# Performance work log

Hardware: AMD Instinct MI355X
Metric: run time of the kernel (lower is better)

The kernel has to match this reference:

```python
import jax, jax.numpy as jnp
import numpy as np

TOP_K = 8
N_GROUP = 8
TOPK_GROUP = 4
ROUTED_SCALING = 2.5
NORM_TOPK_PROB = True


def setup_inputs() -> dict:
    key = jax.random.key(0)
    k1, k2, k3 = jax.random.split(key, 3)
    bsz, seq_len, h = 4, 4096, 4096
    n_experts = 256
    hidden_states = jax.random.normal(k1, (bsz, seq_len, h), dtype=jnp.float32)
    # kaiming_uniform_(a=sqrt(5)) -> uniform(-1/sqrt(h), 1/sqrt(h)) approximately
    bound = 1.0 / np.sqrt(h)
    weight = jax.random.uniform(k2, (n_experts, h), dtype=jnp.float32, minval=-bound, maxval=bound)
    # correction bias is a buffer, zero-init; give it small random values to exercise the path
    e_score_correction_bias = jax.random.normal(k3, (n_experts,), dtype=jnp.float32) * 0.01
    return {"hidden_states": hidden_states, "weight": weight,
            "e_score_correction_bias": e_score_correction_bias}


def reference(hidden_states, weight, e_score_correction_bias):
    bsz, seq_len, h = hidden_states.shape
    n_experts = weight.shape[0]
    x = hidden_states.reshape(-1, h).astype(jnp.float32)          # [N, h]
    logits = jnp.einsum('nh,eh->ne', x, weight.astype(jnp.float32))  # [N, E]
    scores = jax.nn.sigmoid(logits)                                # [N, E]
    scores_for_choice = scores + e_score_correction_bias[None, :]  # [N, E]

    # group-limited routing: score each group by sum of its top-2 expert scores
    grouped = scores_for_choice.reshape(-1, N_GROUP, n_experts // N_GROUP)
    group_scores = jax.lax.top_k(grouped, 2)[0].sum(axis=-1)       # [N, G]
    _, group_idx = jax.lax.top_k(group_scores, TOPK_GROUP)         # [N, Kg]
    group_mask = jax.nn.one_hot(group_idx, N_GROUP, dtype=scores.dtype).sum(axis=1)  # [N, G]
    score_mask = jnp.repeat(group_mask, n_experts // N_GROUP, axis=-1)               # [N, E]

    tmp_scores = jnp.where(score_mask > 0, scores_for_choice, 0.0)
    _, topk_idx = jax.lax.top_k(tmp_scores, TOP_K)                 # [N, K]
    topk_weight = jnp.take_along_axis(scores, topk_idx, axis=1)    # [N, K] (no bias)

    if TOP_K > 1 and NORM_TOPK_PROB:
        denom = topk_weight.sum(axis=-1, keepdims=True) + 1e-20
        topk_weight = topk_weight / denom
    topk_weight = topk_weight * ROUTED_SCALING
    return topk_idx, topk_weight
```

## Files before the change

kernel.cpp:

```cpp
#include <hip/hip_runtime.h>
#include <math.h>

#define NTOK 16384
#define H 4096
#define NE 256
#define EPS_E 1.2e-5f
#define EPS_G 2.4e-5f
#define FIXCAP 1024
#define FLAGCAP 8192

typedef __attribute__((ext_vector_type(8))) short short8;
typedef __attribute__((ext_vector_type(4))) float f32x4;

__device__ __forceinline__ unsigned short f2bf(float x) {
    union { float f; unsigned u; } v; v.f = x;
    unsigned r = v.u + 0x7FFF + ((v.u >> 16) & 1);
    return (unsigned short)(r >> 16);
}
__device__ __forceinline__ float bf2f(unsigned short h) {
    union { float f; unsigned u; } v; v.u = ((unsigned)h) << 16;
    return v.f;
}

__global__ void zero_ws(int* ws) { if (threadIdx.x == 0) ws[0] = 0; }

__global__ __launch_bounds__(256)
void split_w(const float* __restrict__ W, unsigned short* __restrict__ whi,
             unsigned short* __restrict__ wlo)
{
    const int i = (blockIdx.x * 256 + threadIdx.x) * 4;
    float4 w4 = *(const float4*)(W + i);
    const float wv[4] = {w4.x, w4.y, w4.z, w4.w};
    ushort4 hh, ll;
    unsigned short* hp = (unsigned short*)&hh;
    unsigned short* lp = (unsigned short*)&ll;
    #pragma unroll
    for (int j = 0; j < 4; ++j) {
        unsigned short h = f2bf(wv[j]);
        hp[j] = h;
        lp[j] = f2bf(wv[j] - bf2f(h));
    }
    *(ushort4*)(whi + i) = hh;
    *(ushort4*)(wlo + i) = ll;
}

__global__ __launch_bounds__(256, 3)
void gemm3(const float* __restrict__ X, const unsigned short* __restrict__ Whi,
           const unsigned short* __restrict__ Wlo, float* __restrict__ logits,
           int m_base)
{
    __shared__ __align__(16) unsigned short smem[24576];
    unsigned short* Ah = smem;
    unsigned short* Al = smem + 4096;
    unsigned short* Bh = smem + 8192;
    unsigned short* Bl = smem + 16384;

    const int t = threadIdx.x;
    const int lane = t & 63;
    const int w = t >> 6;
    const int wm = w >> 1, wn = w & 1;
    const int fr = lane & 15, fq = lane >> 4;

    const int G = (int)gridDim.x;
    const int swz = (blockIdx.x & 7) * (G >> 3) + (blockIdx.x >> 3);
    const int nb = swz & 1;
    const int mb = swz >> 1;
    const int mloc = mb * 64;
    const int m0 = m_base + mloc;
    const int e0 = nb * 128;

    f32x4 acc[2][4];
    #pragma unroll
    for (int a = 0; a < 2; ++a)
        #pragma unroll
        for (int b = 0; b < 4; ++b) acc[a][b] = (f32x4){0.f, 0.f, 0.f, 0.f};

    const int ar = t >> 2;
    const int akc = t & 3;
    const float* gxa = X + (size_t)(m0 + ar) * H + akc * 16;

    const int blr = lane >> 3;
    const int bsrc = (lane & 7) ^ blr;
    const unsigned short* gbh = Whi + (size_t)(e0 + w * 8 + blr) * H + bsrc * 8;
    const unsigned short* gbl = Wlo + (size_t)(e0 + w * 8 + blr) * H + bsrc * 8;

    float4 xr0, xr1, xr2, xr3;
    auto loadX = [&](int kt) {
        const float* p = gxa + (size_t)kt * 64;
        xr0 = *(const float4*)p;       xr1 = *(const float4*)(p + 4);
        xr2 = *(const float4*)(p + 8); xr3 = *(const float4*)(p + 12);
    };

    loadX(0);

    #pragma unroll 1
    for (int kt = 0; kt < 64; ++kt) {
        __builtin_amdgcn_sched_barrier(0);
        __builtin_amdgcn_s_barrier();
        __builtin_amdgcn_sched_barrier(0);
        const size_t k0 = (size_t)kt * 64;
        #pragma unroll
        for (int i = 0; i < 4; ++i) {
            __builtin_amdgcn_global_load_lds(
                (const __attribute__((address_space(1))) void*)(gbh + (size_t)(32 * i) * H + k0),
                (__attribute__((address_space(3))) void*)&Bh[(w * 8 + 32 * i) * 64], 16, 0, 0);
            __builtin_amdgcn_global_load_lds(
                (const __attribute__((address_space(1))) void*)(gbl + (size_t)(32 * i) * H + k0),
                (__attribute__((address_space(3))) void*)&Bl[(w * 8 + 32 * i) * 64], 16, 0, 0);
        }
        __builtin_amdgcn_sched_barrier(0);
        asm volatile("s_waitcnt vmcnt(8)" ::: "memory");
        __builtin_amdgcn_sched_barrier(0);
        {
            const float xf[16] = {xr0.x, xr0.y, xr0.z, xr0.w, xr1.x, xr1.y, xr1.z, xr1.w,
                                  xr2.x, xr2.y, xr2.z, xr2.w, xr3.x, xr3.y, xr3.z, xr3.w};
            short8 h0, h1, l0, l1;
            #pragma unroll
            for (int j = 0; j < 16; ++j) {
                union { float f; unsigned u; } uu; uu.f = xf[j];
                union { unsigned u; float f; } hh; hh.u = uu.u & 0xFFFF0000u;
                union { float f; unsigned u; } ll; ll.f = xf[j] - hh.f;
                unsigned short hs = (unsigned short)(uu.u >> 16);
                unsigned short ls = (unsigned short)(ll.u >> 16);
                if (j < 8) { h0[j] = (short)hs; l0[j] = (short)ls; }
                else       { h1[j - 8] = (short)hs; l1[j - 8] = (short)ls; }
            }
            const int c0 = akc * 2;
            const int p0 = (c0 ^ (ar & 7)) * 8, p1 = ((c0 + 1) ^ (ar & 7)) * 8;
            *(short8*)&Ah[ar * 64 + p0] = h0;
            *(short8*)&Ah[ar * 64 + p1] = h1;
            *(short8*)&Al[ar * 64 + p0] = l0;
            *(short8*)&Al[ar * 64 + p1] = l1;
        }
        loadX(kt + 1 < 64 ? kt + 1 : 63);
        __builtin_amdgcn_sched_barrier(0);
        asm volatile("s_waitcnt vmcnt(4) lgkmcnt(0)" ::: "memory");
        __builtin_amdgcn_sched_barrier(0);
        __builtin_amdgcn_s_barrier();
        __builtin_amdgcn_sched_barrier(0);
        #pragma unroll
        for (int kk = 0; kk < 2; ++kk) {
            short8 ah[2], al[2], bh[4], bl[4];
            #pragma unroll
            for (int mt = 0; mt < 2; ++mt) {
                const int r = wm * 32 + mt * 16 + fr;
                const int pos = ((kk * 4 + fq) ^ (r & 7)) * 8;
                ah[mt] = *(const short8*)&Ah[r * 64 + pos];
                al[mt] = *(const short8*)&Al[r * 64 + pos];
            }
            #pragma unroll
            for (int nt = 0; nt < 4; ++nt) {
                const int r = wn * 64 + nt * 16 + fr;
                const int pos = ((kk * 4 + fq) ^ (r & 7)) * 8;
                bh[nt] = *(const short8*)&Bh[r * 64 + pos];
                bl[nt] = *(const short8*)&Bl[r * 64 + pos];
            }
            #pragma unroll
            for (int mt = 0; mt < 2; ++mt)
                #pragma unroll
                for (int nt = 0; nt < 4; ++nt)
                    acc[mt][nt] = __builtin_amdgcn_mfma_f32_16x16x32_bf16(ah[mt], bh[nt], acc[mt][nt], 0, 0, 0);
            #pragma unroll
            for (int mt = 0; mt < 2; ++mt)
                #pragma unroll
                for (int nt = 0; nt < 4; ++nt)
                    acc[mt][nt] = __builtin_amdgcn_mfma_f32_16x16x32_bf16(ah[mt], bl[nt], acc[mt][nt], 0, 0, 0);
            #pragma unroll
            for (int mt = 0; mt < 2; ++mt)
                #pragma unroll
                for (int nt = 0; nt < 4; ++nt)
                    acc[mt][nt] = __builtin_amdgcn_mfma_f32_16x16x32_bf16(al[mt], bh[nt], acc[mt][nt], 0, 0, 0);
        }
    }
    asm volatile("" :: "v"(xr0.x), "v"(xr1.x), "v"(xr2.x), "v"(xr3.x));

    #pragma unroll
    for (int mt = 0; mt < 2; ++mt)
        #pragma unroll
        for (int nt = 0; nt < 4; ++nt)
            #pragma unroll
            for (int r = 0; r < 4; ++r)
                logits[(size_t)(mloc + wm * 32 + mt * 16 + fq * 4 + r) * NE +
                       (e0 + wn * 64 + nt * 16 + fr)] = acc[mt][nt][r];
}

__global__ __launch_bounds__(256)
void route(const float* __restrict__ logits, const float* __restrict__ bias,
           float* __restrict__ out, int* __restrict__ ws, int cap, int m_base)
{
    const int t = threadIdx.x, lane = t & 63, wv = t >> 6;
    const float4 bf4 = *(const float4*)(bias + lane * 4);
    const float bfa[4] = {bf4.x, bf4.y, bf4.z, bf4.w};

    #pragma unroll 1
    for (int tt = 0; tt < 8; ++tt) {
        const int local = blockIdx.x * 32 + wv * 8 + tt;
        const int n = m_base + local;
        const float4 lg = *(const float4*)&logits[(size_t)local * NE + lane * 4];
        const float lga[4] = {lg.x, lg.y, lg.z, lg.w};
        float s[4], sc[4];
        #pragma unroll
        for (int i = 0; i < 4; ++i) {
            s[i] = 1.f / (1.f + expf(-lga[i]));
            sc[i] = s[i] + bfa[i];
        }
        float a1 = fmaxf(sc[0], sc[1]), a2 = fminf(sc[0], sc[1]);
        float b1 = fmaxf(sc[2], sc[3]), b2 = fminf(sc[2], sc[3]);
        float t1 = fmaxf(a1, b1);
        float t2 = fmaxf(fminf(a1, b1), fmaxf(a2, b2));
        #pragma unroll
        for (int off = 1; off <= 4; off <<= 1) {
            float o1 = __shfl_xor(t1, off, 64);
            float o2 = __shfl_xor(t2, off, 64);
            float n1 = fmaxf(t1, o1);
            float n2 = fmaxf(fminf(t1, o1), fmaxf(t2, o2));
            t1 = n1; t2 = n2;
        }
        const float gsum = t1 + t2;
        float gsv[8];
        #pragma unroll
        for (int g = 0; g < 8; ++g) gsv[g] = __shfl(gsum, g * 8, 64);

        float minsel = 3e38f, maxuns = -3e38f;
        bool sel = false;
        const int myg = lane >> 3;
        #pragma unroll
        for (int g = 0; g < 8; ++g) {
            int cg = 0;
            #pragma unroll
            for (int g2 = 0; g2 < 8; ++g2)
                cg += (gsv[g2] > gsv[g] || (gsv[g2] == gsv[g] && g2 < g)) ? 1 : 0;
            const bool sg = (cg < 4);
            if (sg) minsel = fminf(minsel, gsv[g]); else maxuns = fmaxf(maxuns, gsv[g]);
            if (myg == g) sel = sg;
        }
        bool flag = (minsel - maxuns) < EPS_G;

        float v[4];
        #pragma unroll
        for (int i = 0; i < 4; ++i) v[i] = sel ? sc[i] : 0.f;

        int idxs[8]; float sigs[8];
        float denom = 0.f, prevv = 0.f;
        #pragma unroll
        for (int r = 0; r < 9; ++r) {
            float bv = v[0]; int bi = 0; float bs = s[0];
            #pragma unroll
            for (int i = 1; i < 4; ++i)
                if (v[i] > bv) { bv = v[i]; bi = i; bs = s[i]; }
            int bidx = (lane << 2) + bi;
            #pragma unroll
            for (int off = 1; off < 64; off <<= 1) {
                float ov = __shfl_xor(bv, off, 64);
                int  oi = __shfl_xor(bidx, off, 64);
                float os = __shfl_xor(bs, off, 64);
                if (ov > bv || (ov == bv && oi < bidx)) { bv = ov; bidx = oi; bs = os; }
            }
            if (r > 0) flag = flag || ((prevv - bv) < EPS_E);
            prevv = bv;
            if (r < 8) {
                idxs[r] = bidx; sigs[r] = bs; denom += bs;
                if ((bidx >> 2) == lane) {
                    #pragma unroll
                    for (int i = 0; i < 4; ++i)
                        if ((bidx & 3) == i) v[i] = -3e38f;
                }
            }
        }
        denom += 1e-20f;
        #pragma unroll
        for (int r = 0; r < 8; ++r)
            if (lane == r) {
                out[n * 8 + r] = (float)idxs[r];
                out[NTOK * 8 + n * 8 + r] = sigs[r] / denom * 2.5f;
            }
        if (flag && lane == 0) {
            int slot = atomicAdd(ws, 1);
            if (slot < cap) ws[16 + slot] = n;
        }
    }
}

__global__ __launch_bounds__(256)
void fix1(const float* __restrict__ X, const float* __restrict__ W,
          const int* __restrict__ ws, double* __restrict__ fixlog, int cap)
{
    __shared__ float Xs4[4][4096];
    const int t = threadIdx.x, lane = t & 63, wv = t >> 6;
    int count = ws[0]; if (count > cap) count = cap;
    const int ngrp = (count + 3) >> 2;

    for (int task = blockIdx.x; task < ngrp * 8; task += (int)gridDim.x) {
        const int g = task >> 3, er = task & 7;
        int tok[4];
        #pragma unroll
        for (int q = 0; q < 4; ++q) {
            const int idx = g * 4 + q;
            tok[q] = ws[16 + (idx < count ? idx : g * 4)];
        }
        __syncthreads();
        #pragma unroll
        for (int q = 0; q < 4; ++q)
            for (int k = t * 4; k < 4096; k += 1024)
                *(float4*)&Xs4[q][k] = *(const float4*)(X + (size_t)tok[q] * H + k);
        __syncthreads();
        #pragma unroll 1
        for (int cc = 0; cc < 2; ++cc) {
            const int eb = er * 32 + wv * 8 + cc * 4;
            double a[4][4];
            #pragma unroll
            for (int q = 0; q < 4; ++q)
                #pragma unroll
                for (int ee = 0; ee < 4; ++ee) a[q][ee] = 0.0;
            for (int j = 0; j < 16; ++j) {
                const int kb = (lane + 64 * j) * 4;
                double xx[4][4];
                #pragma unroll
                for (int q = 0; q < 4; ++q) {
                    float4 x4 = *(const float4*)&Xs4[q][kb];
                    xx[q][0] = x4.x; xx[q][1] = x4.y; xx[q][2] = x4.z; xx[q][3] = x4.w;
                }
                #pragma unroll
                for (int ee = 0; ee < 4; ++ee) {
                    float4 w4 = *(const float4*)(W + (size_t)(eb + ee) * H + kb);
                    const double wd[4] = {w4.x, w4.y, w4.z, w4.w};
                    #pragma unroll
                    for (int q = 0; q < 4; ++q)
                        #pragma unroll
                        for (int kq = 0; kq < 4; ++kq)
                            a[q][ee] = fma(xx[q][kq], wd[kq], a[q][ee]);
                }
            }
            #pragma unroll
            for (int q = 0; q < 4; ++q)
                #pragma unroll
                for (int ee = 0; ee < 4; ++ee) {
                    double v = a[q][ee];
                    #pragma unroll
                    for (int off = 1; off < 64; off <<= 1)
                        v += __shfl_xor(v, off, 64);
                    if (lane == 0) fixlog[(size_t)(g * 4 + q) * NE + eb + ee] = v;
                }
        }
    }
}

__global__ __launch_bounds__(256)
void fix2(const double* __restrict__ fixlog, const float* __restrict__ bias,
          float* __restrict__ out, const int* __restrict__ ws, int cap)
{
    const int t = threadIdx.x, lane = t & 63, wv = t >> 6;
    int count = ws[0]; if (count > cap) count = cap;
    const int ngrp = (count + 3) >> 2;

    for (int g = blockIdx.x; g < ngrp; g += (int)gridDim.x) {
        const int idx = g * 4 + wv;
        const int slot = (idx < count) ? idx : g * 4;
        const int n = ws[16 + slot];
        const double* L = fixlog + (size_t)(g * 4 + wv) * NE;

        double s[4], sc[4];
        #pragma unroll
        for (int ii = 0; ii < 4; ++ii) {
            const double Lv = L[lane * 4 + ii];
            s[ii] = 1.0 / (1.0 + exp(-Lv));
            sc[ii] = s[ii] + (double)bias[lane * 4 + ii];
        }
        double a1 = fmax(sc[0], sc[1]), a2 = fmin(sc[0], sc[1]);
        double b1 = fmax(sc[2], sc[3]), b2 = fmin(sc[2], sc[3]);
        double t1 = fmax(a1, b1);
        double t2 = fmax(fmin(a1, b1), fmax(a2, b2));
        #pragma unroll
        for (int off = 1; off <= 4; off <<= 1) {
            double o1 = __shfl_xor(t1, off, 64);
            double o2 = __shfl_xor(t2, off, 64);
            double n1 = fmax(t1, o1);
            double n2 = fmax(fmin(t1, o1), fmax(t2, o2));
            t1 = n1; t2 = n2;
        }
        const double gsum = t1 + t2;
        double gsv[8];
        #pragma unroll
        for (int gg = 0; gg < 8; ++gg) gsv[gg] = __shfl(gsum, gg * 8, 64);
        const int myg = lane >> 3;
        int cnt = 0;
        #pragma unroll
        for (int gg = 0; gg < 8; ++gg)
            cnt += (gsv[gg] > gsum || (gsv[gg] == gsum && gg < myg)) ? 1 : 0;
        const bool sel = (cnt < 4);

        double v[4];
        #pragma unroll
        for (int ii = 0; ii < 4; ++ii) v[ii] = sel ? sc[ii] : 0.0;

        int idxs[8]; double sigs[8];
        double denom = 0.0;
        #pragma unroll
        for (int r = 0; r < 8; ++r) {
            double bv = v[0]; int bi = 0; double bs = s[0];
            #pragma unroll
            for (int ii = 1; ii < 4; ++ii)
                if (v[ii] > bv) { bv = v[ii]; bi = ii; bs = s[ii]; }
            int bidx = (lane << 2) + bi;
            #pragma unroll
            for (int off = 1; off < 64; off <<= 1) {
                double ov = __shfl_xor(bv, off, 64);
                int oi = __shfl_xor(bidx, off, 64);
                double os = __shfl_xor(bs, off, 64);
                if (ov > bv || (ov == bv && oi < bidx)) { bv = ov; bidx = oi; bs = os; }
            }
            idxs[r] = bidx; sigs[r] = bs; denom += bs;
            if ((bidx >> 2) == lane) {
                #pragma unroll
                for (int ii = 0; ii < 4; ++ii)
                    if ((bidx & 3) == ii) v[ii] = -1.0e300;
            }
        }
        denom += 1e-20;
        #pragma unroll
        for (int r = 0; r < 8; ++r)
            if (lane == r) {
                out[n * 8 + r] = (float)idxs[r];
                out[NTOK * 8 + n * 8 + r] = (float)(sigs[r] / denom * 2.5);
            }
    }
}

__global__ __launch_bounds__(512, 2)
void moe_fused(const float* __restrict__ X, const unsigned short* __restrict__ Whi,
               const unsigned short* __restrict__ Wlo, const float* __restrict__ bias,
               float* __restrict__ out, int* __restrict__ ws, int cap)
{
    __shared__ __align__(16) unsigned short smem[73728];
    unsigned short* xh  = smem;
    unsigned short* xl  = smem + 4096;
    unsigned short* wh0 = smem + 8192;
    unsigned short* wl0 = smem + 24576;
    unsigned short* wh1 = smem + 40960;
    unsigned short* wl1 = smem + 57344;

    const int t = threadIdx.x;
    const int lane = t & 63;
    const int wv = t >> 6;
    const int wr = wv >> 2;
    const int wc = wv & 3;
    const int m0 = blockIdx.x * 64;
    const int fr = lane & 15;
    const int fq = lane >> 4;

    f32x4 acc[2][4];
    #pragma unroll
    for (int a = 0; a < 2; ++a)
        #pragma unroll
        for (int b = 0; b < 4; ++b) acc[a][b] = (f32x4){0.f, 0.f, 0.f, 0.f};

    const int xrow = t >> 3;
    const int xch  = t & 7;
    const int xpos = xch ^ (xrow & 7);
    const float* gx = X + (size_t)(m0 + xrow) * H + xch * 8;

    const int wlr = lane >> 3;
    const int wlc = (lane & 7) ^ wlr;
    const unsigned short* gwh = Whi + (size_t)(wv * 8 + wlr) * H + wlc * 8;
    const unsigned short* gwl = Wlo + (size_t)(wv * 8 + wlr) * H + wlc * 8;

    auto issueW = [&](unsigned short* dh, unsigned short* dl, int kt) {
        const size_t k0 = (size_t)kt * 64;
        #pragma unroll
        for (int i = 0; i < 4; ++i) {
            __builtin_amdgcn_global_load_lds(
                (const __attribute__((address_space(1))) void*)(gwh + (size_t)(64 * i) * H + k0),
                (__attribute__((address_space(3))) void*)&dh[(wv * 8 + 64 * i) * 64], 16, 0, 0);
            __builtin_amdgcn_global_load_lds(
                (const __attribute__((address_space(1))) void*)(gwl + (size_t)(64 * i) * H + k0),
                (__attribute__((address_space(3))) void*)&dl[(wv * 8 + 64 * i) * 64], 16, 0, 0);
        }
    };

    auto kstep = [&](float4& xa, float4& xb, const unsigned short* bufh,
                     const unsigned short* bufl, unsigned short* nbufh,
                     unsigned short* nbufl, int ktw, int ktx) {
        const float xv[8] = {xa.x, xa.y, xa.z, xa.w, xb.x, xb.y, xb.z, xb.w};
        short8 h8, l8;
        #pragma unroll
        for (int j = 0; j < 8; ++j) {
            unsigned short h = f2bf(xv[j]);
// ... 145 lines not shown
                idxs[r] = bidx; sigs[r] = bs; denom += bs;
                if ((bidx >> 2) == lane) {
                    #pragma unroll
                    for (int i = 0; i < 4; ++i)
                        if ((bidx & 3) == i) v[i] = -3e38f;
                }
            }
        }
        denom += 1e-20f;
        const int n = m0 + tok;
        #pragma unroll
        for (int r = 0; r < 8; ++r)
            if (lane == r) {
                out[n * 8 + r] = (float)idxs[r];
                out[NTOK * 8 + n * 8 + r] = sigs[r] / denom * 2.5f;
            }
        if (flag && lane == 0) {
            int slot = atomicAdd(ws, 1);
            if (slot < cap) ws[16 + slot] = n;
        }
    }
}

__global__ __launch_bounds__(256)
void moe_fix(const float* __restrict__ X, const float* __restrict__ W,
             const float* __restrict__ bias, float* __restrict__ out,
             const int* __restrict__ ws, int cap)
{
    __shared__ double Xd[H];
    __shared__ double Ld[NE];
    const int t = threadIdx.x;
    const int lane = t & 63;
    const int wv = t >> 6;
    int count = ws[0]; if (count > cap) count = cap;

    for (int i = blockIdx.x; i < count; i += (int)gridDim.x) {
        const int n = ws[16 + i];
        __syncthreads();
        const float* xrow = X + (size_t)n * H;
        for (int k = t * 4; k < H; k += 1024) {
            float4 x4 = *(const float4*)(xrow + k);
            Xd[k] = (double)x4.x; Xd[k + 1] = (double)x4.y;
            Xd[k + 2] = (double)x4.z; Xd[k + 3] = (double)x4.w;
        }
        __syncthreads();
        #pragma unroll 1
        for (int cc = 0; cc < 16; ++cc) {
            const int e0 = wv * 64 + cc * 4;
            double a[4] = {0.0, 0.0, 0.0, 0.0};
            for (int j = 0; j < 16; ++j) {
                const int kb = (lane + 64 * j) * 4;
                const double x0 = Xd[kb], x1 = Xd[kb + 1], x2 = Xd[kb + 2], x3 = Xd[kb + 3];
                #pragma unroll
                for (int ee = 0; ee < 4; ++ee) {
                    float4 w4 = *(const float4*)(W + (size_t)(e0 + ee) * H + kb);
                    a[ee] = fma(x0, (double)w4.x, a[ee]);
                    a[ee] = fma(x1, (double)w4.y, a[ee]);
                    a[ee] = fma(x2, (double)w4.z, a[ee]);
                    a[ee] = fma(x3, (double)w4.w, a[ee]);
                }
            }
            #pragma unroll
            for (int ee = 0; ee < 4; ++ee)
                #pragma unroll
                for (int off = 1; off < 64; off <<= 1)
                    a[ee] += __shfl_xor(a[ee], off, 64);
            if (lane == 0) { Ld[e0] = a[0]; Ld[e0 + 1] = a[1]; Ld[e0 + 2] = a[2]; Ld[e0 + 3] = a[3]; }
        }
        __syncthreads();
        if (wv == 0) {
            double s[4], sc[4];
            #pragma unroll
            for (int ii = 0; ii < 4; ++ii) {
                const double L = Ld[lane * 4 + ii];
                s[ii] = 1.0 / (1.0 + exp(-L));
                sc[ii] = s[ii] + (double)bias[lane * 4 + ii];
            }
            double a1 = fmax(sc[0], sc[1]), a2 = fmin(sc[0], sc[1]);
            double b1 = fmax(sc[2], sc[3]), b2 = fmin(sc[2], sc[3]);
            double t1 = fmax(a1, b1);
            double t2 = fmax(fmin(a1, b1), fmax(a2, b2));
            #pragma unroll
            for (int off = 1; off <= 4; off <<= 1) {
                double o1 = __shfl_xor(t1, off, 64);
                double o2 = __shfl_xor(t2, off, 64);
                double n1 = fmax(t1, o1);
                double n2 = fmax(fmin(t1, o1), fmax(t2, o2));
                t1 = n1; t2 = n2;
            }
            const double gsum = t1 + t2;
            double gsv[8];
            #pragma unroll
            for (int g = 0; g < 8; ++g) gsv[g] = __shfl(gsum, g * 8, 64);
            const int myg = lane >> 3;
            int cnt = 0;
            #pragma unroll
            for (int g = 0; g < 8; ++g)
                cnt += (gsv[g] > gsum || (gsv[g] == gsum && g < myg)) ? 1 : 0;
            const bool sel = (cnt < 4);
            double v[4];
            #pragma unroll
            for (int ii = 0; ii < 4; ++ii) v[ii] = sel ? sc[ii] : 0.0;
            int idxs[8]; double sigs[8];
            double denom = 0.0;
            #pragma unroll
            for (int r = 0; r < 8; ++r) {
                double bv = v[0]; int bi = 0; double bs = s[0];
                #pragma unroll
                for (int ii = 1; ii < 4; ++ii)
                    if (v[ii] > bv) { bv = v[ii]; bi = ii; bs = s[ii]; }
                int bidx = (lane << 2) + bi;
                #pragma unroll
                for (int off = 1; off < 64; off <<= 1) {
                    double ov = __shfl_xor(bv, off, 64);
                    int oi = __shfl_xor(bidx, off, 64);
                    double os = __shfl_xor(bs, off, 64);
                    if (ov > bv || (ov == bv && oi < bidx)) { bv = ov; bidx = oi; bs = os; }
                }
                idxs[r] = bidx; sigs[r] = bs; denom += bs;
                if ((bidx >> 2) == lane) {
                    #pragma unroll
                    for (int ii = 0; ii < 4; ++ii)
                        if ((bidx & 3) == ii) v[ii] = -1.0e300;
                }
            }
            denom += 1e-20;
            #pragma unroll
            for (int r = 0; r < 8; ++r)
                if (lane == r) {
                    out[n * 8 + r] = (float)idxs[r];
                    out[NTOK * 8 + n * 8 + r] = (float)(sigs[r] / denom * 2.5);
                }
        }
    }
}

#define FXP 34
#define FEP 260
__global__ __launch_bounds__(256)
void moe_fb(const float* __restrict__ X, const float* __restrict__ W,
            const float* __restrict__ bias, float* __restrict__ out)
{
    __shared__ double Xs[16 * FXP];
    __shared__ double Ws[16 * FEP];
    const int t = threadIdx.x;
    const int lane = t & 63;
    const int wv = t >> 6;
    const int m0 = blockIdx.x * 32;
    double acc[8][4];
    #pragma unroll
    for (int i = 0; i < 8; ++i)
        #pragma unroll
        for (int j = 0; j < 4; ++j) acc[i][j] = 0.0;
    const int xm = t >> 3, xk = (t & 7) * 2;
    const int we = t >> 2, wk = (t & 3) * 4;
    const float* gx = X + (size_t)(m0 + xm) * H + xk;
    const float* gw = W + (size_t)we * H + wk;
    float2 xreg = *(const float2*)(gx);
    float4 wreg[4];
    #pragma unroll
    for (int p = 0; p < 4; ++p) wreg[p] = *(const float4*)(gw + (size_t)(64 * p) * H);
    const int NT = H / 16;
    for (int t0 = 0; t0 < NT; ++t0) {
        __syncthreads();
        Xs[(xk + 0) * FXP + xm] = (double)xreg.x;
        Xs[(xk + 1) * FXP + xm] = (double)xreg.y;
        #pragma unroll
        for (int p = 0; p < 4; ++p) {
            const int e = we + 64 * p;
            Ws[(wk + 0) * FEP + e] = (double)wreg[p].x;
            Ws[(wk + 1) * FEP + e] = (double)wreg[p].y;
            Ws[(wk + 2) * FEP + e] = (double)wreg[p].z;
            Ws[(wk + 3) * FEP + e] = (double)wreg[p].w;
        }
        __syncthreads();
        if (t0 + 1 < NT) {
            const int off = (t0 + 1) * 16;
            xreg = *(const float2*)(gx + off);
            #pragma unroll
            for (int p = 0; p < 4; ++p) wreg[p] = *(const float4*)(gw + (size_t)(64 * p) * H + off);
        }
        #pragma unroll
        for (int j = 0; j < 16; ++j) {
            const double* xrow = &Xs[j * FXP + wv * 8];
            const double2 wa = *(const double2*)&Ws[j * FEP + lane * 4];
            const double2 wb = *(const double2*)&Ws[j * FEP + lane * 4 + 2];
            const double ws4[4] = {wa.x, wa.y, wb.x, wb.y};
            #pragma unroll
            for (int mi = 0; mi < 8; ++mi)
                #pragma unroll
                for (int ei = 0; ei < 4; ++ei)
                    acc[mi][ei] = fma(xrow[mi], ws4[ei], acc[mi][ei]);
        }
    }
    const float4 bf = *(const float4*)(bias + lane * 4);
    const double bfa[4] = {(double)bf.x, (double)bf.y, (double)bf.z, (double)bf.w};
    #pragma unroll 1
    for (int tt = 0; tt < 8; ++tt) {
        double s[4], sc[4];
        #pragma unroll
        for (int i = 0; i < 4; ++i) {
            s[i] = 1.0 / (1.0 + exp(-acc[tt][i]));
            sc[i] = s[i] + bfa[i];
        }
        double a1 = fmax(sc[0], sc[1]), a2 = fmin(sc[0], sc[1]);
        double b1 = fmax(sc[2], sc[3]), b2 = fmin(sc[2], sc[3]);
        double t1 = fmax(a1, b1);
        double t2 = fmax(fmin(a1, b1), fmax(a2, b2));
        #pragma unroll
        for (int off = 1; off <= 4; off <<= 1) {
            double o1 = __shfl_xor(t1, off, 64);
            double o2 = __shfl_xor(t2, off, 64);
            double n1 = fmax(t1, o1);
            double n2 = fmax(fmin(t1, o1), fmax(t2, o2));
            t1 = n1; t2 = n2;
        }
        const double gsum = t1 + t2;
        double gsv[8];
        #pragma unroll
        for (int g = 0; g < 8; ++g) gsv[g] = __shfl(gsum, g * 8, 64);
        const int myg = lane >> 3;
        int cnt = 0;
        #pragma unroll
        for (int g = 0; g < 8; ++g)
            cnt += (gsv[g] > gsum || (gsv[g] == gsum && g < myg)) ? 1 : 0;
        const bool sel = (cnt < 4);
        double v[4];
        #pragma unroll
        for (int i = 0; i < 4; ++i) v[i] = sel ? sc[i] : 0.0;
        int idxs[8]; double sigs[8];
        double denom = 0.0;
        #pragma unroll
        for (int r = 0; r < 8; ++r) {
            double bv = v[0]; int bi = 0; double bs = s[0];
            #pragma unroll
            for (int i = 1; i < 4; ++i)
                if (v[i] > bv) { bv = v[i]; bi = i; bs = s[i]; }
            int bidx = (lane << 2) + bi;
            #pragma unroll
            for (int off = 1; off < 64; off <<= 1) {
                double ov = __shfl_xor(bv, off, 64);
                int oi = __shfl_xor(bidx, off, 64);
                double os = __shfl_xor(bs, off, 64);
                if (ov > bv || (ov == bv && oi < bidx)) { bv = ov; bidx = oi; bs = os; }
            }
            idxs[r] = bidx; sigs[r] = bs; denom += bs;
            if ((bidx >> 2) == lane) {
                #pragma unroll
                for (int i = 0; i < 4; ++i)
                    if ((bidx & 3) == i) v[i] = -1.0e300;
            }
        }
        denom += 1e-20;
        const size_t n = (size_t)(m0 + wv * 8 + tt);
        #pragma unroll
        for (int r = 0; r < 8; ++r)
            if (lane == r) {
                out[n * 8 + r] = (float)idxs[r];
                out[(size_t)NTOK * 8 + n * 8 + r] = (float)(sigs[r] / denom * 2.5);
            }
    }
}

extern "C" void kernel_launch(void* const* d_in, const int* in_sizes, int n_in,
                              void* d_out, int out_size, void* d_ws, size_t ws_size,
                              hipStream_t stream) {
    const float* X = (const float*)d_in[0];
    const float* W = (const float*)d_in[1];
    const float* bias = (const float*)d_in[2];
    float* out = (float*)d_out;

    const size_t WB = (size_t)NE * H * 2;
    const size_t OFF_W = 65536;
    const size_t OFF_FIX = OFF_W + 2 * WB;
    const size_t FIXB = (size_t)FIXCAP * NE * 8;
    const size_t OFF_LOG = OFF_FIX + FIXB;
    const size_t NEED1 = OFF_FIX;
    const size_t minlog = (size_t)256 * NE * 4;

    if (ws_size < NEED1) {
        moe_fb<<<NTOK / 32, 256, 0, stream>>>(X, W, bias, out);
        return;
    }
    int* ws = (int*)d_ws;
    unsigned short* whi = (unsigned short*)((char*)d_ws + OFF_W);
    unsigned short* wlo = whi + (size_t)NE * H;

    zero_ws<<<1, 64, 0, stream>>>(ws);
    split_w<<<(NE * H) / 1024, 256, 0, stream>>>(W, whi, wlo);

    if (ws_size >= OFF_LOG + minlog) {
        double* fixlog = (double*)((char*)d_ws + OFF_FIX);
        float* logits = (float*)((char*)d_ws + OFF_LOG);
        const size_t avail = ws_size - OFF_LOG;
        size_t full = (size_t)NTOK * NE * 4;
        int CT;
        if (avail >= full) CT = NTOK;
        else {
            CT = (int)(avail / ((size_t)NE * 4));
            CT &= ~255;
        }
        for (int mb0 = 0; mb0 < NTOK; mb0 += CT) {
            int ct = (NTOK - mb0 < CT) ? (NTOK - mb0) : CT;
            gemm3<<<(ct / 64) * 2, 256, 0, stream>>>(X, whi, wlo, logits, mb0);
            route<<<ct / 32, 256, 0, stream>>>(logits, bias, out, ws, FLAGCAP, mb0);
        }
        fix1<<<2048, 256, 0, stream>>>(X, W, ws, fixlog, FIXCAP);
        fix2<<<256, 256, 0, stream>>>(fixlog, bias, out, ws, FIXCAP);
    } else {
        moe_fused<<<NTOK / 64, 512, 0, stream>>>(X, whi, wlo, bias, out, ws, FLAGCAP);
        moe_fix<<<1024, 256, 0, stream>>>(X, W, bias, out, ws, FLAGCAP);
    }
}
```

Baseline: 223.8 us.

## Double-buffer weight tiles in LDS with K=32 steps and MFMA priority boost

Restructures the split-bf16 GEMM main loop. K-tiles shrink from 64 to 32 and the B (weight hi/lo) tiles are double-buffered in LDS, so the next tile's global_load_lds runs while MFMAs consume the current one. The A tile gets a padded row stride of 40 instead of an XOR swizzle, B gets a new XOR swizzle, and s_setprio raises wave priority around the MFMA block. In exchange there are twice as many iterations and barriers, and the hand-tuned vmcnt counts must match the new load pattern exactly.

Result: slower. 263.9 us (+17.9%).

```diff
diff --git a/kernel.cpp b/kernel.cpp
--- a/kernel.cpp
+++ b/kernel.cpp
@@ -49,11 +49,13 @@
            const unsigned short* __restrict__ Wlo, float* __restrict__ logits,
            int m_base)
 {
-    __shared__ __align__(16) unsigned short smem[24576];
-    unsigned short* Ah = smem;
-    unsigned short* Al = smem + 4096;
-    unsigned short* Bh = smem + 8192;
-    unsigned short* Bl = smem + 16384;
+    __shared__ __align__(16) unsigned short smem[21504];
+    unsigned short* Bh0 = smem;
+    unsigned short* Bl0 = smem + 4096;
+    unsigned short* Bh1 = smem + 8192;
+    unsigned short* Bl1 = smem + 12288;
+    unsigned short* Ah  = smem + 16384;
+    unsigned short* Al  = smem + 18944;
 
     const int t = threadIdx.x;
     const int lane = t & 63;
@@ -76,103 +78,114 @@
         for (int b = 0; b < 4; ++b) acc[a][b] = (f32x4){0.f, 0.f, 0.f, 0.f};
 
     const int ar = t >> 2;
-    const int akc = t & 3;
-    const float* gxa = X + (size_t)(m0 + ar) * H + akc * 16;
-
-    const int blr = lane >> 3;
-    const int bsrc = (lane & 7) ^ blr;
-    const unsigned short* gbh = Whi + (size_t)(e0 + w * 8 + blr) * H + bsrc * 8;
-    const unsigned short* gbl = Wlo + (size_t)(e0 + w * 8 + blr) * H + bsrc * 8;
-
-    float4 xr0, xr1, xr2, xr3;
+    const int ac = t & 3;
+    const float* gxa = X + (size_t)(m0 + ar) * H + ac * 8;
+
+    const int srcc = (lane & 3) ^ ((lane >> 3) & 3);
+    const unsigned short* gbh = Whi + (size_t)(e0 + w * 32 + (lane >> 2)) * H + srcc * 8;
+    const unsigned short* gbl = Wlo + (size_t)(e0 + w * 32 + (lane >> 2)) * H + srcc * 8;
+
+    auto issueB = [&](unsigned short* dh, unsigned short* dl, int kt) {
+        const size_t k0 = (size_t)kt * 32;
+        #pragma unroll
+        for (int i = 0; i < 2; ++i) {
+            __builtin_amdgcn_global_load_lds(
+                (const __attribute__((address_space(1))) void*)(gbh + (size_t)(16 * i) * H + k0),
+                (__attribute__((address_space(3))) void*)&dh[(w * 32 + 16 * i) * 32], 16, 0, 0);
+            __builtin_amdgcn_global_load_lds(
+                (const __attribute__((address_space(1))) void*)(gbl + (size_t)(16 * i) * H + k0),
+                (__attribute__((address_space(3))) void*)&dl[(w * 32 + 16 * i) * 32], 16, 0, 0);
+        }
+    };
+
+    float4 xr0, xr1;
     auto loadX = [&](int kt) {
-        const float* p = gxa + (size_t)kt * 64;
-        xr0 = *(const float4*)p;       xr1 = *(const float4*)(p + 4);
-        xr2 = *(const float4*)(p + 8); xr3 = *(const float4*)(p + 12);
+        const float* p = gxa + (size_t)kt * 32;
+        xr0 = *(const float4*)p;
+        xr1 = *(const float4*)(p + 4);
     };
 
-    loadX(0);
-
-    #pragma unroll 1
-    for (int kt = 0; kt < 64; ++kt) {
-        __builtin_amdgcn_sched_barrier(0);
-        __builtin_amdgcn_s_barrier();
-        __builtin_amdgcn_sched_barrier(0);
-        const size_t k0 = (size_t)kt * 64;
-        #pragma unroll
-        for (int i = 0; i < 4; ++i) {
-            __builtin_amdgcn_global_load_lds(
-                (const __attribute__((address_space(1))) void*)(gbh + (size_t)(32 * i) * H + k0),
-                (__attribute__((address_space(3))) void*)&Bh[(w * 8 + 32 * i) * 64], 16, 0, 0);
-            __builtin_amdgcn_global_load_lds(
-                (const __attribute__((address_space(1))) void*)(gbl + (size_t)(32 * i) * H + k0),
-                (__attribute__((address_space(3))) void*)&Bl[(w * 8 + 32 * i) * 64], 16, 0, 0);
-        }
-        __builtin_amdgcn_sched_barrier(0);
-        asm volatile("s_waitcnt vmcnt(8)" ::: "memory");
+    const int apos = fq * 8;
+    const int bpos = (fq ^ ((fr >> 1) & 3)) * 8;
+
+    auto step = [&](const unsigned short* Bhc, const unsigned short* Blc,
+                    unsigned short* Bhn, unsigned short* Bln, int kt) {
+        issueB(Bhn, Bln, (kt + 1) & 127);
+        __builtin_amdgcn_sched_barrier(0);
+        asm volatile("s_waitcnt vmcnt(16)" ::: "memory");
         __builtin_amdgcn_sched_barrier(0);
         {
-            const float xf[16] = {xr0.x, xr0.y, xr0.z, xr0.w, xr1.x, xr1.y, xr1.z, xr1.w,
-                                  xr2.x, xr2.y, xr2.z, xr2.w, xr3.x, xr3.y, xr3.z, xr3.w};
-            short8 h0, h1, l0, l1;
-            #pragma unroll
-            for (int j = 0; j < 16; ++j) {
+            const float xf[8] = {xr0.x, xr0.y, xr0.z, xr0.w, xr1.x, xr1.y, xr1.z, xr1.w};
+            short8 h8, l8;
+            #pragma unroll
+            for (int j = 0; j < 8; ++j) {
                 union { float f; unsigned u; } uu; uu.f = xf[j];
                 union { unsigned u; float f; } hh; hh.u = uu.u & 0xFFFF0000u;
                 union { float f; unsigned u; } ll; ll.f = xf[j] - hh.f;
-                unsigned short hs = (unsigned short)(uu.u >> 16);
-                unsigned short ls = (unsigned short)(ll.u >> 16);
-                if (j < 8) { h0[j] = (short)hs; l0[j] = (short)ls; }
-                else       { h1[j - 8] = (short)hs; l1[j - 8] = (short)ls; }
-            }
-            const int c0 = akc * 2;
-            const int p0 = (c0 ^ (ar & 7)) * 8, p1 = ((c0 + 1) ^ (ar & 7)) * 8;
-            *(short8*)&Ah[ar * 64 + p0] = h0;
-            *(short8*)&Ah[ar * 64 + p1] = h1;
-            *(short8*)&Al[ar * 64 + p0] = l0;
-            *(short8*)&Al[ar * 64 + p1] = l1;
-        }
-        loadX(kt + 1 < 64 ? kt + 1 : 63);
-        __builtin_amdgcn_sched_barrier(0);
-        asm volatile("s_waitcnt vmcnt(4) lgkmcnt(0)" ::: "memory");
+                h8[j] = (short)(uu.u >> 16);
+                l8[j] = (short)(ll.u >> 16);
+            }
+            *(short8*)&Ah[ar * 40 + ac * 8] = h8;
+            *(short8*)&Al[ar * 40 + ac * 8] = l8;
+        }
+        loadX(kt + 1 < 128 ? kt + 1 : 127);
+        __builtin_amdgcn_sched_barrier(0);
+        asm volatile("s_waitcnt lgkmcnt(0)" ::: "memory");
         __builtin_amdgcn_sched_barrier(0);
         __builtin_amdgcn_s_barrier();
         __builtin_amdgcn_sched_barrier(0);
-        #pragma unroll
-        for (int kk = 0; kk < 2; ++kk) {
-            short8 ah[2], al[2], bh[4], bl[4];
-            #pragma unroll
-            for (int mt = 0; mt < 2; ++mt) {
-                const int r = wm * 32 + mt * 16 + fr;
-                const int pos = ((kk * 4 + fq) ^ (r & 7)) * 8;
-                ah[mt] = *(const short8*)&Ah[r * 64 + pos];
-                al[mt] = *(const short8*)&Al[r * 64 + pos];
-            }
-            #pragma unroll
-            for (int nt = 0; nt < 4; ++nt) {
-                const int r = wn * 64 + nt * 16 + fr;
-                const int pos = ((kk * 4 + fq) ^ (r & 7)) * 8;
-                bh[nt] = *(const short8*)&Bh[r * 64 + pos];
-                bl[nt] = *(const short8*)&Bl[r * 64 + pos];
-            }
-            #pragma unroll
-            for (int mt = 0; mt < 2; ++mt)
-                #pragma unroll
-                for (int nt = 0; nt < 4; ++nt)
-                    acc[mt][nt] = __builtin_amdgcn_mfma_f32_16x16x32_bf16(ah[mt], bh[nt], acc[mt][nt], 0, 0, 0);
-            #pragma unroll
-            for (int mt = 0; mt < 2; ++mt)
-                #pragma unroll
-                for (int nt = 0; nt < 4; ++nt)
-                    acc[mt][nt] = __builtin_amdgcn_mfma_f32_16x16x32_bf16(ah[mt], bl[nt], acc[mt][nt], 0, 0, 0);
-            #pragma unroll
-            for (int mt = 0; mt < 2; ++mt)
-                #pragma unroll
-                for (int nt = 0; nt < 4; ++nt)
-                    acc[mt][nt] = __builtin_amdgcn_mfma_f32_16x16x32_bf16(al[mt], bh[nt], acc[mt][nt], 0, 0, 0);
-        }
-    }
-    asm volatile("" :: "v"(xr0.x), "v"(xr1.x), "v"(xr2.x), "v"(xr3.x));
+        short8 ah[2], al[2], bh[4], bl[4];
+        #pragma unroll
+        for (int mt = 0; mt < 2; ++mt) {
+            const int r = wm * 32 + mt * 16 + fr;
+            ah[mt] = *(const short8*)&Ah[r * 40 + apos];
+            al[mt] = *(const short8*)&Al[r * 40 + apos];
+        }
+        #pragma unroll
+        for (int nt = 0; nt < 4; ++nt) {
+            const int rb = wn * 64 + nt * 16 + fr;
+            bh[nt] = *(const short8*)&Bhc[rb * 32 + bpos];
+            bl[nt] = *(const short8*)&Blc[rb * 32 + bpos];
+        }
+        __builtin_amdgcn_s_setprio(1);
+        #pragma unroll
+        for (int mt = 0; mt < 2; ++mt)
+            #pragma unroll
+            for (int nt = 0; nt < 4; ++nt)
+                acc[mt][nt] = __builtin_amdgcn_mfma_f32_16x16x32_bf16(ah[mt], bh[nt], acc[mt][nt], 0, 0, 0);
+        #pragma unroll
+        for (int mt = 0; mt < 2; ++mt)
+            #pragma unroll
+            for (int nt = 0; nt < 4; ++nt)
+                acc[mt][nt] = __builtin_amdgcn_mfma_f32_16x16x32_bf16(ah[mt], bl[nt], acc[mt][nt], 0, 0, 0);
+        #pragma unroll
+        for (int mt = 0; mt < 2; ++mt)
+            #pragma unroll
+            for (int nt = 0; nt < 4; ++nt)
+                acc[mt][nt] = __builtin_amdgcn_mfma_f32_16x16x32_bf16(al[mt], bh[nt], acc[mt][nt], 0, 0, 0);
+        __builtin_amdgcn_s_setprio(0);
+        __builtin_amdgcn_sched_barrier(0);
+        asm volatile("s_waitcnt vmcnt(2) lgkmcnt(0)" ::: "memory");
+        __builtin_amdgcn_sched_barrier(0);
+        __builtin_amdgcn_s_barrier();
+    };
+
+    issueB(Bh0, Bl0, 0);
+    __builtin_amdgcn_sched_barrier(0);
+    loadX(0);
+    __builtin_amdgcn_sched_barrier(0);
+    asm volatile("s_waitcnt vmcnt(2)" ::: "memory");
+    __builtin_amdgcn_sched_barrier(0);
+    __builtin_amdgcn_s_barrier();
+
+    #pragma unroll 1
+    for (int kt = 0; kt < 128; kt += 2) {
+        step(Bh0, Bl0, Bh1, Bl1, kt);
+        step(Bh1, Bl1, Bh0, Bl0, kt + 1);
+    }
+    asm volatile("" :: "v"(xr0.x), "v"(xr0.y), "v"(xr0.z), "v"(xr0.w),
+                       "v"(xr1.x), "v"(xr1.y), "v"(xr1.z), "v"(xr1.w));
+    asm volatile("s_waitcnt vmcnt(0) lgkmcnt(0)" ::: "memory");
 
     #pragma unroll
     for (int mt = 0; mt < 2; ++mt)
```

## Double-buffer W tiles in LDS and prefetch next k-tile during MFMA

Applied to the files above, without the earlier changes.

Splits the B (weight hi/lo) shared-memory tiles into two buffers so the global-to-LDS loads for tile k+1 are issued while tile k is consumed. All LDS fragments are read into registers before a barrier, and the MFMA chain then runs at raised wave priority. This is meant to hide global load latency behind compute. In exchange LDS use grows from 48 KB to 80 KB, the occupancy hint drops from 3 to 2 blocks per CU, and register pressure rises from holding both k-slices of fragments.

Result: slower. 232.7 us (+4.0%).

```diff
diff --git a/kernel.cpp b/kernel.cpp
--- a/kernel.cpp
+++ b/kernel.cpp
@@ -44,16 +44,18 @@
     *(ushort4*)(wlo + i) = ll;
 }
 
-__global__ __launch_bounds__(256, 3)
+__global__ __launch_bounds__(256, 2)
 void gemm3(const float* __restrict__ X, const unsigned short* __restrict__ Whi,
            const unsigned short* __restrict__ Wlo, float* __restrict__ logits,
            int m_base)
 {
-    __shared__ __align__(16) unsigned short smem[24576];
-    unsigned short* Ah = smem;
-    unsigned short* Al = smem + 4096;
-    unsigned short* Bh = smem + 8192;
-    unsigned short* Bl = smem + 16384;
+    __shared__ __align__(16) unsigned short smem[40960];
+    unsigned short* Bh0 = smem;
+    unsigned short* Bl0 = smem + 8192;
+    unsigned short* Bh1 = smem + 16384;
+    unsigned short* Bl1 = smem + 24576;
+    unsigned short* Ah  = smem + 32768;
+    unsigned short* Al  = smem + 36864;
 
     const int t = threadIdx.x;
     const int lane = t & 63;
@@ -84,6 +86,19 @@
     const unsigned short* gbh = Whi + (size_t)(e0 + w * 8 + blr) * H + bsrc * 8;
     const unsigned short* gbl = Wlo + (size_t)(e0 + w * 8 + blr) * H + bsrc * 8;
 
+    auto issueB = [&](unsigned short* dh, unsigned short* dl, int kt) {
+        const size_t k0 = (size_t)kt * 64;
+        #pragma unroll
+        for (int i = 0; i < 4; ++i) {
+            __builtin_amdgcn_global_load_lds(
+                (const __attribute__((address_space(1))) void*)(gbh + (size_t)(32 * i) * H + k0),
+                (__attribute__((address_space(3))) void*)&dh[(w * 8 + 32 * i) * 64], 16, 0, 0);
+            __builtin_amdgcn_global_load_lds(
+                (const __attribute__((address_space(1))) void*)(gbl + (size_t)(32 * i) * H + k0),
+                (__attribute__((address_space(3))) void*)&dl[(w * 8 + 32 * i) * 64], 16, 0, 0);
+        }
+    };
+
     float4 xr0, xr1, xr2, xr3;
     auto loadX = [&](int kt) {
         const float* p = gxa + (size_t)kt * 64;
@@ -91,23 +106,9 @@
         xr2 = *(const float4*)(p + 8); xr3 = *(const float4*)(p + 12);
     };
 
-    loadX(0);
-
-    #pragma unroll 1
-    for (int kt = 0; kt < 64; ++kt) {
-        __builtin_amdgcn_sched_barrier(0);
-        __builtin_amdgcn_s_barrier();
-        __builtin_amdgcn_sched_barrier(0);
-        const size_t k0 = (size_t)kt * 64;
-        #pragma unroll
-        for (int i = 0; i < 4; ++i) {
-            __builtin_amdgcn_global_load_lds(
-                (const __attribute__((address_space(1))) void*)(gbh + (size_t)(32 * i) * H + k0),
-                (__attribute__((address_space(3))) void*)&Bh[(w * 8 + 32 * i) * 64], 16, 0, 0);
-            __builtin_amdgcn_global_load_lds(
-                (const __attribute__((address_space(1))) void*)(gbl + (size_t)(32 * i) * H + k0),
-                (__attribute__((address_space(3))) void*)&Bl[(w * 8 + 32 * i) * 64], 16, 0, 0);
-        }
+    auto step = [&](const unsigned short* Bhc, const unsigned short* Blc,
+                    unsigned short* Bhn, unsigned short* Bln, int kt) {
+        issueB(Bhn, Bln, (kt + 1) & 63);
         __builtin_amdgcn_sched_barrier(0);
         asm volatile("s_waitcnt vmcnt(8)" ::: "memory");
         __builtin_amdgcn_sched_barrier(0);
@@ -134,45 +135,69 @@
         }
         loadX(kt + 1 < 64 ? kt + 1 : 63);
         __builtin_amdgcn_sched_barrier(0);
-        asm volatile("s_waitcnt vmcnt(4) lgkmcnt(0)" ::: "memory");
+        asm volatile("s_waitcnt lgkmcnt(0)" ::: "memory");
         __builtin_amdgcn_sched_barrier(0);
         __builtin_amdgcn_s_barrier();
         __builtin_amdgcn_sched_barrier(0);
+        short8 ah[2][2], al[2][2], bh[2][4], bl[2][4];
         #pragma unroll
         for (int kk = 0; kk < 2; ++kk) {
-            short8 ah[2], al[2], bh[4], bl[4];
             #pragma unroll
             for (int mt = 0; mt < 2; ++mt) {
                 const int r = wm * 32 + mt * 16 + fr;
                 const int pos = ((kk * 4 + fq) ^ (r & 7)) * 8;
-                ah[mt] = *(const short8*)&Ah[r * 64 + pos];
-                al[mt] = *(const short8*)&Al[r * 64 + pos];
+                ah[kk][mt] = *(const short8*)&Ah[r * 64 + pos];
+                al[kk][mt] = *(const short8*)&Al[r * 64 + pos];
             }
             #pragma unroll
             for (int nt = 0; nt < 4; ++nt) {
                 const int r = wn * 64 + nt * 16 + fr;
                 const int pos = ((kk * 4 + fq) ^ (r & 7)) * 8;
-                bh[nt] = *(const short8*)&Bh[r * 64 + pos];
-                bl[nt] = *(const short8*)&Bl[r * 64 + pos];
-            }
+                bh[kk][nt] = *(const short8*)&Bhc[r * 64 + pos];
+                bl[kk][nt] = *(const short8*)&Blc[r * 64 + pos];
+            }
+        }
+        asm volatile("s_waitcnt lgkmcnt(0)" ::: "memory");
+        __builtin_amdgcn_sched_barrier(0);
+        __builtin_amdgcn_s_barrier();
+        __builtin_amdgcn_sched_barrier(0);
+        __builtin_amdgcn_s_setprio(1);
+        #pragma unroll
+        for (int kk = 0; kk < 2; ++kk)
             #pragma unroll
             for (int mt = 0; mt < 2; ++mt)
                 #pragma unroll
                 for (int nt = 0; nt < 4; ++nt)
-                    acc[mt][nt] = __builtin_amdgcn_mfma_f32_16x16x32_bf16(ah[mt], bh[nt], acc[mt][nt], 0, 0, 0);
+                    acc[mt][nt] = __builtin_amdgcn_mfma_f32_16x16x32_bf16(ah[kk][mt], bh[kk][nt], acc[mt][nt], 0, 0, 0);
+        #pragma unroll
+        for (int kk = 0; kk < 2; ++kk)
             #pragma unroll
             for (int mt = 0; mt < 2; ++mt)
                 #pragma unroll
                 for (int nt = 0; nt < 4; ++nt)
-                    acc[mt][nt] = __builtin_amdgcn_mfma_f32_16x16x32_bf16(ah[mt], bl[nt], acc[mt][nt], 0, 0, 0);
+                    acc[mt][nt] = __builtin_amdgcn_mfma_f32_16x16x32_bf16(ah[kk][mt], bl[kk][nt], acc[mt][nt], 0, 0, 0);
+        #pragma unroll
+        for (int kk = 0; kk < 2; ++kk)
             #pragma unroll
             for (int mt = 0; mt < 2; ++mt)
                 #pragma unroll
                 for (int nt = 0; nt < 4; ++nt)
-                    acc[mt][nt] = __builtin_amdgcn_mfma_f32_16x16x32_bf16(al[mt], bh[nt], acc[mt][nt], 0, 0, 0);
-        }
+                    acc[mt][nt] = __builtin_amdgcn_mfma_f32_16x16x32_bf16(al[kk][mt], bh[kk][nt], acc[mt][nt], 0, 0, 0);
+        __builtin_amdgcn_s_setprio(0);
+    };
+
+    issueB(Bh0, Bl0, 0);
+    __builtin_amdgcn_sched_barrier(0);
+    loadX(0);
+    __builtin_amdgcn_sched_barrier(0);
+
+    #pragma unroll 1
+    for (int kt = 0; kt < 64; kt += 2) {
+        step(Bh0, Bl0, Bh1, Bl1, kt);
+        step(Bh1, Bl1, Bh0, Bl0, kt + 1);
     }
     asm volatile("" :: "v"(xr0.x), "v"(xr1.x), "v"(xr2.x), "v"(xr3.x));
+    asm volatile("s_waitcnt vmcnt(0) lgkmcnt(0)" ::: "memory");
 
     #pragma unroll
     for (int mt = 0; mt < 2; ++mt)
```

## Shrink GEMM block tile to 32 rows and raise occupancy to 4 blocks

Applied to the files above, without the earlier changes.

Halves the M tile of the split-bf16 router GEMM from 64 to 32 tokens per block and lays out the four waves along N, each covering 32 experts. The grid doubles, LDS per block shrinks, and launch bounds request four blocks per CU instead of three. The loop barriers are also reworked so each iteration ends with a wait and barrier after the MFMAs rather than starting with one. The intent is more parallelism and better latency hiding on a memory-bound GEMM, at the cost of reading the W tiles twice as often per token and lowering arithmetic intensity.

Result: slower. 256.8 us (+14.8%).

```diff
diff --git a/kernel.cpp b/kernel.cpp
--- a/kernel.cpp
+++ b/kernel.cpp
@@ -44,60 +44,47 @@
     *(ushort4*)(wlo + i) = ll;
 }
 
-__global__ __launch_bounds__(256, 3)
+__global__ __launch_bounds__(256, 4)
 void gemm3(const float* __restrict__ X, const unsigned short* __restrict__ Whi,
            const unsigned short* __restrict__ Wlo, float* __restrict__ logits,
            int m_base)
 {
-    __shared__ __align__(16) unsigned short smem[24576];
-    unsigned short* Ah = smem;
-    unsigned short* Al = smem + 4096;
-    unsigned short* Bh = smem + 8192;
-    unsigned short* Bl = smem + 16384;
+    __shared__ __align__(16) unsigned short smem[20480];
+    unsigned short* Bh = smem;
+    unsigned short* Bl = smem + 8192;
+    unsigned short* Ah = smem + 16384;
+    unsigned short* Al = smem + 18432;
 
     const int t = threadIdx.x;
     const int lane = t & 63;
     const int w = t >> 6;
-    const int wm = w >> 1, wn = w & 1;
     const int fr = lane & 15, fq = lane >> 4;
 
     const int G = (int)gridDim.x;
     const int swz = (blockIdx.x & 7) * (G >> 3) + (blockIdx.x >> 3);
     const int nb = swz & 1;
     const int mb = swz >> 1;
-    const int mloc = mb * 64;
+    const int mloc = mb * 32;
     const int m0 = m_base + mloc;
     const int e0 = nb * 128;
 
-    f32x4 acc[2][4];
+    f32x4 acc[2][2];
     #pragma unroll
     for (int a = 0; a < 2; ++a)
         #pragma unroll
-        for (int b = 0; b < 4; ++b) acc[a][b] = (f32x4){0.f, 0.f, 0.f, 0.f};
-
-    const int ar = t >> 2;
-    const int akc = t & 3;
-    const float* gxa = X + (size_t)(m0 + ar) * H + akc * 16;
+        for (int b = 0; b < 2; ++b) acc[a][b] = (f32x4){0.f, 0.f, 0.f, 0.f};
+
+    const int ar = t >> 3;
+    const int ac = t & 7;
+    const int apos = (ac ^ (ar & 7)) * 8;
+    const float* gxa = X + (size_t)(m0 + ar) * H + ac * 8;
 
     const int blr = lane >> 3;
     const int bsrc = (lane & 7) ^ blr;
     const unsigned short* gbh = Whi + (size_t)(e0 + w * 8 + blr) * H + bsrc * 8;
     const unsigned short* gbl = Wlo + (size_t)(e0 + w * 8 + blr) * H + bsrc * 8;
 
-    float4 xr0, xr1, xr2, xr3;
-    auto loadX = [&](int kt) {
-        const float* p = gxa + (size_t)kt * 64;
-        xr0 = *(const float4*)p;       xr1 = *(const float4*)(p + 4);
-        xr2 = *(const float4*)(p + 8); xr3 = *(const float4*)(p + 12);
-    };
-
-    loadX(0);
-
-    #pragma unroll 1
-    for (int kt = 0; kt < 64; ++kt) {
-        __builtin_amdgcn_sched_barrier(0);
-        __builtin_amdgcn_s_barrier();
-        __builtin_amdgcn_sched_barrier(0);
+    auto issueB = [&](int kt) {
         const size_t k0 = (size_t)kt * 64;
         #pragma unroll
         for (int i = 0; i < 4; ++i) {
@@ -108,49 +95,56 @@
                 (const __attribute__((address_space(1))) void*)(gbl + (size_t)(32 * i) * H + k0),
                 (__attribute__((address_space(3))) void*)&Bl[(w * 8 + 32 * i) * 64], 16, 0, 0);
         }
+    };
+
+    float4 xr0, xr1;
+    auto loadX = [&](int kt) {
+        const float* p = gxa + (size_t)kt * 64;
+        xr0 = *(const float4*)p;
+        xr1 = *(const float4*)(p + 4);
+    };
+
+    loadX(0);
+    __builtin_amdgcn_sched_barrier(0);
+
+    #pragma unroll 1
+    for (int kt = 0; kt < 64; ++kt) {
+        issueB(kt);
         __builtin_amdgcn_sched_barrier(0);
         asm volatile("s_waitcnt vmcnt(8)" ::: "memory");
         __builtin_amdgcn_sched_barrier(0);
         {
-            const float xf[16] = {xr0.x, xr0.y, xr0.z, xr0.w, xr1.x, xr1.y, xr1.z, xr1.w,
-                                  xr2.x, xr2.y, xr2.z, xr2.w, xr3.x, xr3.y, xr3.z, xr3.w};
-            short8 h0, h1, l0, l1;
-            #pragma unroll
-            for (int j = 0; j < 16; ++j) {
+            const float xf[8] = {xr0.x, xr0.y, xr0.z, xr0.w, xr1.x, xr1.y, xr1.z, xr1.w};
+            short8 h8, l8;
+            #pragma unroll
+            for (int j = 0; j < 8; ++j) {
                 union { float f; unsigned u; } uu; uu.f = xf[j];
                 union { unsigned u; float f; } hh; hh.u = uu.u & 0xFFFF0000u;
                 union { float f; unsigned u; } ll; ll.f = xf[j] - hh.f;
-                unsigned short hs = (unsigned short)(uu.u >> 16);
-                unsigned short ls = (unsigned short)(ll.u >> 16);
-                if (j < 8) { h0[j] = (short)hs; l0[j] = (short)ls; }
-                else       { h1[j - 8] = (short)hs; l1[j - 8] = (short)ls; }
-            }
-            const int c0 = akc * 2;
-            const int p0 = (c0 ^ (ar & 7)) * 8, p1 = ((c0 + 1) ^ (ar & 7)) * 8;
-            *(short8*)&Ah[ar * 64 + p0] = h0;
-            *(short8*)&Ah[ar * 64 + p1] = h1;
-            *(short8*)&Al[ar * 64 + p0] = l0;
-            *(short8*)&Al[ar * 64 + p1] = l1;
+                h8[j] = (short)(uu.u >> 16);
+                l8[j] = (short)(ll.u >> 16);
+            }
+            *(short8*)&Ah[ar * 64 + apos] = h8;
+            *(short8*)&Al[ar * 64 + apos] = l8;
         }
         loadX(kt + 1 < 64 ? kt + 1 : 63);
         __builtin_amdgcn_sched_barrier(0);
-        asm volatile("s_waitcnt vmcnt(4) lgkmcnt(0)" ::: "memory");
+        asm volatile("s_waitcnt vmcnt(2) lgkmcnt(0)" ::: "memory");
         __builtin_amdgcn_sched_barrier(0);
         __builtin_amdgcn_s_barrier();
-        __builtin_amdgcn_sched_barrier(0);
         #pragma unroll
         for (int kk = 0; kk < 2; ++kk) {
-            short8 ah[2], al[2], bh[4], bl[4];
+            short8 ah[2], al[2], bh[2], bl[2];
             #pragma unroll
             for (int mt = 0; mt < 2; ++mt) {
-                const int r = wm * 32 + mt * 16 + fr;
+                const int r = mt * 16 + fr;
                 const int pos = ((kk * 4 + fq) ^ (r & 7)) * 8;
                 ah[mt] = *(const short8*)&Ah[r * 64 + pos];
                 al[mt] = *(const short8*)&Al[r * 64 + pos];
             }
             #pragma unroll
-            for (int nt = 0; nt < 4; ++nt) {
-                const int r = wn * 64 + nt * 16 + fr;
+            for (int nt = 0; nt < 2; ++nt) {
+                const int r = w * 32 + nt * 16 + fr;
                 const int pos = ((kk * 4 + fq) ^ (r & 7)) * 8;
                 bh[nt] = *(const short8*)&Bh[r * 64 + pos];
                 bl[nt] = *(const short8*)&Bl[r * 64 + pos];
@@ -158,30 +152,36 @@
             #pragma unroll
             for (int mt = 0; mt < 2; ++mt)
                 #pragma unroll
-                for (int nt = 0; nt < 4; ++nt)
+                for (int nt = 0; nt < 2; ++nt)
                     acc[mt][nt] = __builtin_amdgcn_mfma_f32_16x16x32_bf16(ah[mt], bh[nt], acc[mt][nt], 0, 0, 0);
             #pragma unroll
             for (int mt = 0; mt < 2; ++mt)
                 #pragma unroll
-                for (int nt = 0; nt < 4; ++nt)
+                for (int nt = 0; nt < 2; ++nt)
                     acc[mt][nt] = __builtin_amdgcn_mfma_f32_16x16x32_bf16(ah[mt], bl[nt], acc[mt][nt], 0, 0, 0);
             #pragma unroll
             for (int mt = 0; mt < 2; ++mt)
                 #pragma unroll
-                for (int nt = 0; nt < 4; ++nt)
+                for (int nt = 0; nt < 2; ++nt)
                     acc[mt][nt] = __builtin_amdgcn_mfma_f32_16x16x32_bf16(al[mt], bh[nt], acc[mt][nt], 0, 0, 0);
         }
-    }
-    asm volatile("" :: "v"(xr0.x), "v"(xr1.x), "v"(xr2.x), "v"(xr3.x));
+        __builtin_amdgcn_sched_barrier(0);
+        asm volatile("s_waitcnt lgkmcnt(0)" ::: "memory");
+        __builtin_amdgcn_sched_barrier(0);
+        __builtin_amdgcn_s_barrier();
+    }
+    asm volatile("" :: "v"(xr0.x), "v"(xr0.y), "v"(xr0.z), "v"(xr0.w),
+                       "v"(xr1.x), "v"(xr1.y), "v"(xr1.z), "v"(xr1.w));
+    asm volatile("s_waitcnt vmcnt(0) lgkmcnt(0)" ::: "memory");
 
     #pragma unroll
     for (int mt = 0; mt < 2; ++mt)
         #pragma unroll
-        for (int nt = 0; nt < 4; ++nt)
+        for (int nt = 0; nt < 2; ++nt)
             #pragma unroll
             for (int r = 0; r < 4; ++r)
-                logits[(size_t)(mloc + wm * 32 + mt * 16 + fq * 4 + r) * NE +
-                       (e0 + wn * 64 + nt * 16 + fr)] = acc[mt][nt][r];
+                logits[(size_t)(mloc + mt * 16 + fq * 4 + r) * NE +
+                       (e0 + w * 32 + nt * 16 + fr)] = acc[mt][nt][r];
 }
 
 __global__ __launch_bounds__(256)
@@ -933,7 +933,7 @@
         }
         for (int mb0 = 0; mb0 < NTOK; mb0 += CT) {
             int ct = (NTOK - mb0 < CT) ? (NTOK - mb0) : CT;
-            gemm3<<<(ct / 64) * 2, 256, 0, stream>>>(X, whi, wlo, logits, mb0);
+            gemm3<<<(ct / 32) * 2, 256, 0, stream>>>(X, whi, wlo, logits, mb0);
             route<<<ct / 32, 256, 0, stream>>>(logits, bias, out, ws, FLAGCAP, mb0);
         }
         fix1<<<2048, 256, 0, stream>>>(X, W, ws, fixlog, FIXCAP);
```
